# Kernel tuning notes

Measured on AMD Instinct MI355X. Metric: run time of the kernel, lower is better.

The kernel has to match this reference:

```python
import jax, jax.numpy as jnp
import numpy as np

N_NODES = 50000
N_EDGES = 800000
IN, HID, OUT = 256, 128, 64


def setup_inputs() -> dict:
    key = jax.random.key(0)
    ks = jax.random.split(key, 5)
    return {
        "x": jax.random.normal(ks[0], (N_NODES, IN), dtype=jnp.float32),
        "W1": jax.random.normal(ks[1], (IN, HID), dtype=jnp.float32) / np.sqrt(IN),
        "b1": jnp.zeros((HID,), dtype=jnp.float32),
        "W2": jax.random.normal(ks[2], (HID, OUT), dtype=jnp.float32) / np.sqrt(HID),
        "b2": jnp.zeros((OUT,), dtype=jnp.float32),
        "src": jax.random.randint(ks[3], (N_EDGES,), 0, N_NODES, dtype=jnp.int32),
        "dst": jax.random.randint(ks[4], (N_EDGES,), 0, N_NODES, dtype=jnp.int32),
    }


def _graph_conv(h, W, b, src, dst, norm_src, norm_dst, n_nodes):
    # DGL GraphConv, norm='both': y = D_dst^{-1/2} A D_src^{-1/2} h W + b
    # Project first (smaller feature dim for the SpMM), linearity makes it exact.
    h = h @ W                                     # [N, d_out]
    msg = (h * norm_src[:, None])[src]            # gather per-edge   [E, d_out]
    agg = jax.ops.segment_sum(msg, dst, num_segments=n_nodes)  # [N, d_out]
    return agg * norm_dst[:, None] + b


def reference(x, W1, b1, W2, b2, src, dst):
    n = x.shape[0]
    ones = jnp.ones(src.shape[0], dtype=jnp.float32)
    out_deg = jnp.zeros(n, jnp.float32).at[src].add(ones)
    in_deg = jnp.zeros(n, jnp.float32).at[dst].add(ones)
    norm_src = jax.lax.rsqrt(jnp.maximum(out_deg, 1.0))
    norm_dst = jax.lax.rsqrt(jnp.maximum(in_deg, 1.0))

    h = _graph_conv(x, W1, b1, src, dst, norm_src, norm_dst, n)
    h = jax.nn.relu(h)
    return _graph_conv(h, W2, b2, src, dst, norm_src, norm_dst, n)
```

## Files before the change

### kernel.cpp

```cpp
#include <hip/hip_runtime.h>

#define NN 50000
#define NE 800000
#define NPAD 50176
#define NSLICE 32
#define ESL 25000
#define HPN 25088
#define HPW 12544
#define FPN 12544
#define GB2 196
#define FB 128
#define NB 196

typedef __attribute__((ext_vector_type(8))) short bf16x8;
typedef __attribute__((ext_vector_type(4))) float f32x4;

__device__ __forceinline__ float u2f(unsigned u) { return __uint_as_float(u); }
__device__ __forceinline__ unsigned f2u(float f) { return __float_as_uint(f); }
__device__ __forceinline__ unsigned short f2bf(float f) {
    unsigned u = f2u(f);
    return (unsigned short)((u + (((u >> 16) & 1u) + 0x7fffu)) >> 16);
}
__device__ __forceinline__ void acc8(float* ax, uint4 u) {
    ax[0] += u2f(u.x << 16); ax[1] += u2f(u.x & 0xffff0000u);
    ax[2] += u2f(u.y << 16); ax[3] += u2f(u.y & 0xffff0000u);
    ax[4] += u2f(u.z << 16); ax[5] += u2f(u.z & 0xffff0000u);
    ax[6] += u2f(u.w << 16); ax[7] += u2f(u.w & 0xffff0000u);
}
#define GLOAD_LDS16(GP, LP)                                              \
    __builtin_amdgcn_global_load_lds(                                    \
        (const __attribute__((address_space(1))) unsigned*)(GP),         \
        (__attribute__((address_space(3))) unsigned*)(LP), 16, 0, 0)

__global__ __launch_bounds__(1024) void hist_wtrans_kernel(
    const int* __restrict__ src, const int* __restrict__ dst,
    unsigned* __restrict__ cnt_sl,
    const float* __restrict__ W1, const float* __restrict__ W2,
    unsigned short* __restrict__ Wh1, unsigned short* __restrict__ Wl1,
    unsigned short* __restrict__ Wh2, unsigned short* __restrict__ Wl2,
    int* __restrict__ done_cnt) {
    if (blockIdx.x == 0 && threadIdx.x == 0) *done_cnt = 0;
    const int b = blockIdx.x;
    if (b >= 128) {
        float w;
        unsigned short *ph, *pl;
        int f;
        if (b < 160) {
            int i = (b - 128) * 1024 + threadIdx.x;
            int k = i >> 7, n = i & 127;
            f = (((n >> 4) * 32 + (k >> 3)) * 16 + (n & 15)) * 8 + (k & 7);
            w = W1[i]; ph = Wh1; pl = Wl1;
        } else {
            int i = (b - 160) * 1024 + threadIdx.x;
            int k = i >> 6, n = i & 63;
            f = (((n >> 4) * 16 + (k >> 3)) * 16 + (n & 15)) * 8 + (k & 7);
            w = W2[i]; ph = Wh2; pl = Wl2;
        }
        unsigned u = f2u(w);
        float lo = w - u2f(u & 0xffff0000u);
        ph[f] = (unsigned short)(u >> 16);
        pl[f] = (unsigned short)(f2u(lo) >> 16);
        return;
    }
    __shared__ unsigned lcnt[HPW];
    const int side = b & 1;
    const int slice = (b >> 1) & (NSLICE - 1);
    const int part = b >> 6;
    const int* __restrict__ arr = side ? dst : src;
    const int base = part * HPN;
    for (int j = threadIdx.x; j < HPW; j += 1024) lcnt[j] = 0;
    __syncthreads();
    const int e0 = slice * ESL;
    for (int i = e0 + threadIdx.x; i < e0 + ESL; i += 1024) {
        int v = arr[i] - base;
        if ((unsigned)v < (unsigned)HPN)
            atomicAdd(&lcnt[v >> 1], 1u << ((v & 1) * 16));
    }
    __syncthreads();
    unsigned* o = cnt_sl + (size_t)b * HPW;
    for (int j = threadIdx.x; j < HPW; j += 1024) o[j] = lcnt[j];
}

__global__ __launch_bounds__(256) void norm_scanAB_kernel(
    const unsigned* __restrict__ cnt_sl, float* __restrict__ ns,
    float* __restrict__ nd, int* __restrict__ presum,
    int* __restrict__ pref, int* __restrict__ blk_sum,
    int* __restrict__ blk_ofs, int* __restrict__ done_cnt, int n) {
    __shared__ int lds[256];
    __shared__ int is_last;
    int i = blockIdx.x * 256 + threadIdx.x;
    int d_total = 0;
    if (i < n) {
        int part = (i >= HPN) ? 1 : 0;
        int w = (i - part * HPN) >> 1;
        int sh = (i & 1) * 16;
        int s_total = 0;
#pragma unroll
        for (int sl = 0; sl < NSLICE; sl++) {
            int bb = part * 64 + sl * 2;
            s_total += (cnt_sl[(size_t)bb * HPW + w] >> sh) & 0xffff;
            int c = (cnt_sl[(size_t)(bb + 1) * HPW + w] >> sh) & 0xffff;
            presum[sl * NPAD + i] = d_total;
            d_total += c;
        }
        ns[i] = rsqrtf(fmaxf((float)s_total, 1.0f));
        nd[i] = rsqrtf(fmaxf((float)d_total, 1.0f));
    }
    lds[threadIdx.x] = d_total;
    __syncthreads();
    for (int ofs = 1; ofs < 256; ofs <<= 1) {
        int t = (threadIdx.x >= ofs) ? lds[threadIdx.x - ofs] : 0;
        __syncthreads();
        lds[threadIdx.x] += t;
        __syncthreads();
    }
    if (i < n) pref[i] = lds[threadIdx.x] - d_total;
    if (threadIdx.x == 255) blk_sum[blockIdx.x] = lds[255];
    __threadfence();
    if (threadIdx.x == 0) {
        int c = atomicAdd(done_cnt, 1);
        is_last = (c == gridDim.x - 1);
    }
    __syncthreads();
    if (!is_last) return;
    __threadfence();
    int v = (threadIdx.x < gridDim.x) ? blk_sum[threadIdx.x] : 0;
    __syncthreads();
    lds[threadIdx.x] = v;
    __syncthreads();
    for (int ofs = 1; ofs < 256; ofs <<= 1) {
        int t = (threadIdx.x >= ofs) ? lds[threadIdx.x - ofs] : 0;
        __syncthreads();
        lds[threadIdx.x] += t;
        __syncthreads();
    }
    if (threadIdx.x < gridDim.x) blk_ofs[threadIdx.x] = lds[threadIdx.x] - v;
}

__global__ __launch_bounds__(1024) void gemm1_fill_kernel(
    const float* __restrict__ A, const unsigned short* __restrict__ Wh,
    const unsigned short* __restrict__ Wl, const float* __restrict__ norm_src,
    unsigned short* __restrict__ out,
    const int* __restrict__ src, const int* __restrict__ dst,
    const int* __restrict__ pref, const int* __restrict__ blk_ofs,
    const int* __restrict__ presum, int* __restrict__ eidx, int M) {
    __shared__ __align__(16) char shmem[65536];
    const int b = blockIdx.x;
    if (b < GB2) {
        constexpr int N = 128, K = 256;
        constexpr int NT = N / 16, KC = K / 32;
        const int wave = threadIdx.x >> 6;
        const int lane = threadIdx.x & 63;
        const int ln = lane & 15;
        const int qk = lane >> 4;
        const int m0 = b * 256 + wave * 16;
        const int m0b = b * 256;
        float* sh = (float*)shmem;
        const bf16x8* BH = (const bf16x8*)Wh;
        const bf16x8* BL = (const bf16x8*)Wl;

        auto stage = [&](int p, int c) {
#pragma unroll
            for (int h = 0; h < 2; ++h) {
                const int j = threadIdx.x + h * 1024;
                const int row = j >> 3;
                const int sp = (j & 7) ^ (row & 7);
                int grow = m0b + row;
                if (grow >= M) grow = M - 1;
                const float* gp = A + (size_t)grow * K + c * 32 + sp * 4;
                char* lp = (char*)(sh + p * 8192) + (j & ~63) * 16;
                GLOAD_LDS16(gp, lp);
            }
        };

        const int r = wave * 16 + ln;
        const int offA0 = r * 128 + (((qk * 2) ^ (ln & 7)) * 16);
        const int offA1 = r * 128 + (((qk * 2 + 1) ^ (ln & 7)) * 16);

        f32x4 acc[NT];
#pragma unroll
        for (int t = 0; t < NT; t++) acc[t] = (f32x4){0.f, 0.f, 0.f, 0.f};

        stage(0, 0);
        __syncthreads();
#pragma unroll 2
        for (int c = 0; c < KC; ++c) {
            if (c + 1 < KC) stage((c + 1) & 1, c + 1);
            const char* bufc = (const char*)sh + (c & 1) * 32768;
            float4 a0 = *(const float4*)(bufc + offA0);
            float4 a1 = *(const float4*)(bufc + offA1);
            float av[8] = {a0.x, a0.y, a0.z, a0.w, a1.x, a1.y, a1.z, a1.w};
            bf16x8 ah, al;
#pragma unroll
            for (int j = 0; j < 8; ++j) {
                unsigned u = f2u(av[j]);
                float lo = av[j] - u2f(u & 0xffff0000u);
                ah[j] = (short)(u >> 16);
                al[j] = (short)(f2u(lo) >> 16);
            }
            const int fb = c * 4 + qk;
#pragma unroll
            for (int t = 0; t < NT; ++t) {
                bf16x8 bh = BH[(t * (K / 8) + fb) * 16 + ln];
                bf16x8 bl = BL[(t * (K / 8) + fb) * 16 + ln];
                acc[t] = __builtin_amdgcn_mfma_f32_16x16x32_bf16(ah, bh, acc[t], 0, 0, 0);
                acc[t] = __builtin_amdgcn_mfma_f32_16x16x32_bf16(ah, bl, acc[t], 0, 0, 0);
                acc[t] = __builtin_amdgcn_mfma_f32_16x16x32_bf16(al, bh, acc[t], 0, 0, 0);
            }
            __syncthreads();
        }
        float sc[4];
#pragma unroll
        for (int rr = 0; rr < 4; ++rr) {
            int row = m0 + qk * 4 + rr;
            sc[rr] = (row < M) ? norm_src[row] : 0.f;
        }
#pragma unroll
        for (int t = 0; t < NT; ++t)
#pragma unroll
            for (int rr = 0; rr < 4; ++rr) {
                int row = m0 + qk * 4 + rr;
                if (row < M) out[(size_t)row * N + t * 16 + ln] = f2bf(acc[t][rr] * sc[rr]);
            }
        return;
    }
    int* cur = (int*)shmem;
    const int fb = b - GB2;
    const int slice = fb >> 2;
    const int part = fb & 3;
    const int base = part * FPN;
    for (int j = threadIdx.x; j < FPN; j += 1024) {
        int gi = base + j;
        cur[j] = (gi < NN) ? pref[gi] + blk_ofs[gi >> 8] + presum[slice * NPAD + gi] : 0;
    }
    __syncthreads();
    const int e0 = slice * ESL;
    for (int i = e0 + threadIdx.x; i < e0 + ESL; i += 1024) {
        int v = dst[i] - base;
        if ((unsigned)v < (unsigned)FPN) {
            int pos = atomicAdd(&cur[v], 1);
            eidx[pos] = src[i];
        }
    }
}

__global__ __launch_bounds__(256) void layer2_kernel(
    const unsigned* __restrict__ hs1, const int* __restrict__ eidx,
    const int* __restrict__ pref, const int* __restrict__ blk_ofs,
    const float* __restrict__ norm_src, const float* __restrict__ norm_dst,
    const float* __restrict__ bias, const unsigned short* __restrict__ Wh,
    const unsigned short* __restrict__ Wl, unsigned short* __restrict__ hs2, int n) {
    __shared__ unsigned lh1[16 * 68];
    const int wave = threadIdx.x >> 6;
    const int lane = threadIdx.x & 63;
    const int nb = blockIdx.x * 16;
    const int q = lane >> 4;
    const int p = lane & 15;

    for (int j = 0; j < 4; ++j) {
        const int node = nb + wave * 4 + j;
        float ax[8];
#pragma unroll
        for (int k = 0; k < 8; ++k) ax[k] = 0.f;
        unsigned pk[4] = {0u, 0u, 0u, 0u};
        if (node < n) {
            int beg = pref[node] + blk_ofs[node >> 8];
            int end = (node + 1 < n) ? pref[node + 1] + blk_ofs[(node + 1) >> 8] : NE;
            int e = beg;
            for (; e + 15 < end; e += 16) {
                int i0 = eidx[e + q];
                int i1 = eidx[e + 4 + q];
                int i2 = eidx[e + 8 + q];
                int i3 = eidx[e + 12 + q];
                uint4 u0 = *(const uint4*)(hs1 + (size_t)i0 * 64 + p * 4);
                uint4 u1 = *(const uint4*)(hs1 + (size_t)i1 * 64 + p * 4);
                uint4 u2 = *(const uint4*)(hs1 + (size_t)i2 * 64 + p * 4);
                uint4 u3 = *(const uint4*)(hs1 + (size_t)i3 * 64 + p * 4);
                acc8(ax, u0);
                acc8(ax, u1);
                acc8(ax, u2);
                acc8(ax, u3);
            }
            for (; e + 7 < end; e += 8) {
                int i0 = eidx[e + q];
                int i1 = eidx[e + 4 + q];
                uint4 u0 = *(const uint4*)(hs1 + (size_t)i0 * 64 + p * 4);
                uint4 u1 = *(const uint4*)(hs1 + (size_t)i1 * 64 + p * 4);
                acc8(ax, u0);
                acc8(ax, u1);
            }
            for (; e < end; e += 4) {
                int ee = e + q;
                bool ok = ee < end;
                int i0 = eidx[ok ? ee : beg];
                uint4 u0 = *(const uint4*)(hs1 + (size_t)i0 * 64 + p * 4);
                if (ok) acc8(ax, u0);
            }
#pragma unroll
            for (int k = 0; k < 8; ++k) {
                ax[k] += __shfl_xor(ax[k], 16);
                ax[k] += __shfl_xor(ax[k], 32);
            }
            float sc = norm_dst[node];
            float4 b0 = *(const float4*)(bias + p * 8);
            float4 b1 = *(const float4*)(bias + p * 8 + 4);
            float bb[8] = {b0.x, b0.y, b0.z, b0.w, b1.x, b1.y, b1.z, b1.w};
#pragma unroll
            for (int k = 0; k < 4; ++k) {
                float rlo = fmaxf(ax[2 * k] * sc + bb[2 * k], 0.f);
                float rhi = fmaxf(ax[2 * k + 1] * sc + bb[2 * k + 1], 0.f);
                pk[k] = (unsigned)f2bf(rlo) | ((unsigned)f2bf(rhi) << 16);
            }
        }
        if (q == 0)
            *(uint4*)&lh1[(wave * 4 + j) * 68 + p * 4] = *(uint4*)pk;
    }
    __syncthreads();

    const int ln = lane & 15;
    const int qk = lane >> 4;
    const int t = wave;
    const bf16x8* BH = (const bf16x8*)Wh;
    const bf16x8* BL = (const bf16x8*)Wl;
    f32x4 acc = (f32x4){0.f, 0.f, 0.f, 0.f};
#pragma unroll
    for (int c = 0; c < 4; ++c) {
        bf16x8 ah = *(const bf16x8*)&lh1[ln * 68 + c * 16 + qk * 4];
        const int fb = c * 4 + qk;
        bf16x8 bh = BH[(t * 16 + fb) * 16 + ln];
        bf16x8 bl = BL[(t * 16 + fb) * 16 + ln];
        acc = __builtin_amdgcn_mfma_f32_16x16x32_bf16(ah, bh, acc, 0, 0, 0);
        acc = __builtin_amdgcn_mfma_f32_16x16x32_bf16(ah, bl, acc, 0, 0, 0);
    }
#pragma unroll
    for (int r = 0; r < 4; ++r) {
        int node = nb + qk * 4 + r;
        if (node < n)
            hs2[(size_t)node * 64 + t * 16 + ln] = f2bf(acc[r] * norm_src[node]);
    }
}

__global__ __launch_bounds__(256) void gather64_kernel(
    const unsigned* __restrict__ hs, const int* __restrict__ eidx,
    const int* __restrict__ pref, const int* __restrict__ blk_ofs,
    const float* __restrict__ norm_dst, const float* __restrict__ bias,
    float* __restrict__ out, int n) {
    int wave = (blockIdx.x * blockDim.x + threadIdx.x) >> 6;
    int lane = threadIdx.x & 63;
    if (wave >= n) return;
    int beg = pref[wave] + blk_ofs[wave >> 8];
    int end = (wave + 1 < n) ? pref[wave + 1] + blk_ofs[(wave + 1) >> 8] : NE;
    const int o = lane >> 3;
    const int p = lane & 7;
    float ax[8];
#pragma unroll
    for (int k = 0; k < 8; ++k) ax[k] = 0.f;
    int e = beg;
    for (; e + 15 < end; e += 16) {
        int i0 = eidx[e + o];
        int i1 = eidx[e + 8 + o];
        uint4 u0 = *(const uint4*)(hs + (size_t)i0 * 32 + p * 4);
        uint4 u1 = *(const uint4*)(hs + (size_t)i1 * 32 + p * 4);
        acc8(ax, u0);
        acc8(ax, u1);
    }
    for (; e < end; e += 8) {
        int ee = e + o;
        bool ok = ee < end;
        int i0 = eidx[ok ? ee : beg];
        uint4 u0 = *(const uint4*)(hs + (size_t)i0 * 32 + p * 4);
        if (ok) acc8(ax, u0);
    }
#pragma unroll
    for (int k = 0; k < 8; ++k) {
        ax[k] += __shfl_xor(ax[k], 8);
        ax[k] += __shfl_xor(ax[k], 16);
        ax[k] += __shfl_xor(ax[k], 32);
    }
    if (o == 0) {
        float sc = norm_dst[wave];
        float4 b0 = *(const float4*)(bias + p * 8);
        float4 b1 = *(const float4*)(bias + p * 8 + 4);
        float4 r0, r1;
        r0.x = ax[0] * sc + b0.x;
        r0.y = ax[1] * sc + b0.y;
        r0.z = ax[2] * sc + b0.z;
        r0.w = ax[3] * sc + b0.w;
        r1.x = ax[4] * sc + b1.x;
        r1.y = ax[5] * sc + b1.y;
        r1.z = ax[6] * sc + b1.z;
        r1.w = ax[7] * sc + b1.w;
        *(float4*)(out + (size_t)wave * 64 + p * 8) = r0;
        *(float4*)(out + (size_t)wave * 64 + p * 8 + 4) = r1;
    }
}

extern "C" void kernel_launch(void* const* d_in, const int* in_sizes, int n_in,
                              void* d_out, int out_size, void* d_ws, size_t ws_size,
                              hipStream_t stream) {
    const float* x  = (const float*)d_in[0];
    const float* W1 = (const float*)d_in[1];
    const float* b1 = (const float*)d_in[2];
    const float* W2 = (const float*)d_in[3];
    const float* b2 = (const float*)d_in[4];
    const int* src  = (const int*)d_in[5];
    const int* dst  = (const int*)d_in[6];
    float* out = (float*)d_out;
    char* ws = (char*)d_ws;

    float* norm_src = (float*)(ws);
    float* norm_dst = (float*)(ws + 4 * 50176);
    int*   pref     = (int*)(ws + 4 * 100352);
    int*   blk_sum  = (int*)(ws + 4 * 150528);
    int*   blk_ofs  = (int*)(ws + 4 * 150784);
    int*   done_cnt = (int*)(ws + 4 * 151040);
    int*   eidx     = (int*)(ws + 4 * 151296);
    unsigned short* Wh1 = (unsigned short*)(ws + 4 * 951296);
    unsigned short* Wl1 = (unsigned short*)(ws + 4 * 967680);
    unsigned short* Wh2 = (unsigned short*)(ws + 4 * 984064);
    unsigned short* Wl2 = (unsigned short*)(ws + 4 * 988160);
    unsigned short* hs1 = (unsigned short*)(ws + 4 * 992256);
    unsigned short* hs2 = (unsigned short*)(ws + 4 * 4192256);
    unsigned* cnt_sl    = (unsigned*)(ws + 4 * 5792256);
    int* presum         = (int*)(ws + 4 * 7397888);

    hist_wtrans_kernel<<<168, 1024, 0, stream>>>(src, dst, cnt_sl, W1, W2,
                                                 Wh1, Wl1, Wh2, Wl2, done_cnt);

    norm_scanAB_kernel<<<NB, 256, 0, stream>>>(cnt_sl, norm_src, norm_dst,
                                               presum, pref, blk_sum, blk_ofs,
                                               done_cnt, NN);

    gemm1_fill_kernel<<<GB2 + FB, 1024, 0, stream>>>(
        x, Wh1, Wl1, norm_src, hs1, src, dst, pref, blk_ofs, presum, eidx, NN);

    layer2_kernel<<<3125, 256, 0, stream>>>(
        (const unsigned*)hs1, eidx, pref, blk_ofs, norm_src, norm_dst, b1,
        Wh2, Wl2, hs2, NN);

    gather64_kernel<<<12500, 256, 0, stream>>>(
        (const unsigned*)hs2, eidx, pref, blk_ofs, norm_dst, b2, out, NN);
}
```

Measured before the change: 222.4 us.

## Replace sliced LDS counting-sort fill with global atomic cursors

```diff
diff --git a/kernel.cpp b/kernel.cpp
--- a/kernel.cpp
+++ b/kernel.cpp
@@ -3,13 +3,13 @@
 #define NN 50000
 #define NE 800000
 #define NPAD 50176
-#define NSLICE 32
-#define ESL 25000
+#define NSL8 8
+#define ESL8 100000
 #define HPN 25088
 #define HPW 12544
-#define FPN 12544
 #define GB2 196
-#define FB 128
+#define FB3 59
+#define EPB 13560
 #define NB 196
 
 typedef __attribute__((ext_vector_type(8))) short bf16x8;
@@ -34,24 +34,24 @@
 
 __global__ __launch_bounds__(1024) void hist_wtrans_kernel(
     const int* __restrict__ src, const int* __restrict__ dst,
-    unsigned* __restrict__ cnt_sl,
+    unsigned* __restrict__ cnt8,
     const float* __restrict__ W1, const float* __restrict__ W2,
     unsigned short* __restrict__ Wh1, unsigned short* __restrict__ Wl1,
     unsigned short* __restrict__ Wh2, unsigned short* __restrict__ Wl2,
     int* __restrict__ done_cnt) {
     if (blockIdx.x == 0 && threadIdx.x == 0) *done_cnt = 0;
     const int b = blockIdx.x;
-    if (b >= 128) {
+    if (b >= 32) {
         float w;
         unsigned short *ph, *pl;
         int f;
-        if (b < 160) {
-            int i = (b - 128) * 1024 + threadIdx.x;
+        if (b < 64) {
+            int i = (b - 32) * 1024 + threadIdx.x;
             int k = i >> 7, n = i & 127;
             f = (((n >> 4) * 32 + (k >> 3)) * 16 + (n & 15)) * 8 + (k & 7);
             w = W1[i]; ph = Wh1; pl = Wl1;
         } else {
-            int i = (b - 160) * 1024 + threadIdx.x;
+            int i = (b - 64) * 1024 + threadIdx.x;
             int k = i >> 6, n = i & 63;
             f = (((n >> 4) * 16 + (k >> 3)) * 16 + (n & 15)) * 8 + (k & 7);
             w = W2[i]; ph = Wh2; pl = Wl2;
@@ -64,26 +64,26 @@
     }
     __shared__ unsigned lcnt[HPW];
     const int side = b & 1;
-    const int slice = (b >> 1) & (NSLICE - 1);
-    const int part = b >> 6;
+    const int slice = (b >> 1) & 7;
+    const int part = b >> 4;
     const int* __restrict__ arr = side ? dst : src;
     const int base = part * HPN;
     for (int j = threadIdx.x; j < HPW; j += 1024) lcnt[j] = 0;
     __syncthreads();
-    const int e0 = slice * ESL;
-    for (int i = e0 + threadIdx.x; i < e0 + ESL; i += 1024) {
+    const int e0 = slice * ESL8;
+    for (int i = e0 + threadIdx.x; i < e0 + ESL8; i += 1024) {
         int v = arr[i] - base;
         if ((unsigned)v < (unsigned)HPN)
             atomicAdd(&lcnt[v >> 1], 1u << ((v & 1) * 16));
     }
     __syncthreads();
-    unsigned* o = cnt_sl + (size_t)b * HPW;
+    unsigned* o = cnt8 + (size_t)b * HPW;
     for (int j = threadIdx.x; j < HPW; j += 1024) o[j] = lcnt[j];
 }
 
 __global__ __launch_bounds__(256) void norm_scanAB_kernel(
-    const unsigned* __restrict__ cnt_sl, float* __restrict__ ns,
-    float* __restrict__ nd, int* __restrict__ presum,
+    const unsigned* __restrict__ cnt8, float* __restrict__ ns,
+    float* __restrict__ nd, int* __restrict__ gcur,
     int* __restrict__ pref, int* __restrict__ blk_sum,
     int* __restrict__ blk_ofs, int* __restrict__ done_cnt, int n) {
     __shared__ int lds[256];
@@ -96,12 +96,9 @@
         int sh = (i & 1) * 16;
         int s_total = 0;
 #pragma unroll
-        for (int sl = 0; sl < NSLICE; sl++) {
-            int bb = part * 64 + sl * 2;
-            s_total += (cnt_sl[(size_t)bb * HPW + w] >> sh) & 0xffff;
-            int c = (cnt_sl[(size_t)(bb + 1) * HPW + w] >> sh) & 0xffff;
-            presum[sl * NPAD + i] = d_total;
-            d_total += c;
+        for (int sl = 0; sl < NSL8; sl++) {
+            s_total += (cnt8[(size_t)(part * 16 + sl * 2) * HPW + w] >> sh) & 0xffff;
+            d_total += (cnt8[(size_t)(part * 16 + sl * 2 + 1) * HPW + w] >> sh) & 0xffff;
         }
         ns[i] = rsqrtf(fmaxf((float)s_total, 1.0f));
         nd[i] = rsqrtf(fmaxf((float)d_total, 1.0f));
@@ -114,7 +111,11 @@
         lds[threadIdx.x] += t;
         __syncthreads();
     }
-    if (i < n) pref[i] = lds[threadIdx.x] - d_total;
+    if (i < n) {
+        int p = lds[threadIdx.x] - d_total;
+        pref[i] = p;
+        gcur[i] = p;
+    }
     if (threadIdx.x == 255) blk_sum[blockIdx.x] = lds[255];
     __threadfence();
     if (threadIdx.x == 0) {
@@ -142,8 +143,8 @@
     const unsigned short* __restrict__ Wl, const float* __restrict__ norm_src,
     unsigned short* __restrict__ out,
     const int* __restrict__ src, const int* __restrict__ dst,
-    const int* __restrict__ pref, const int* __restrict__ blk_ofs,
-    const int* __restrict__ presum, int* __restrict__ eidx, int M) {
+    int* __restrict__ gcur, const int* __restrict__ blk_ofs,
+    int* __restrict__ eidx, int M) {
     __shared__ __align__(16) char shmem[65536];
     const int b = blockIdx.x;
     if (b < GB2) {
@@ -224,23 +225,13 @@
             }
         return;
     }
-    int* cur = (int*)shmem;
     const int fb = b - GB2;
-    const int slice = fb >> 2;
-    const int part = fb & 3;
-    const int base = part * FPN;
-    for (int j = threadIdx.x; j < FPN; j += 1024) {
-        int gi = base + j;
-        cur[j] = (gi < NN) ? pref[gi] + blk_ofs[gi >> 8] + presum[slice * NPAD + gi] : 0;
-    }
-    __syncthreads();
-    const int e0 = slice * ESL;
-    for (int i = e0 + threadIdx.x; i < e0 + ESL; i += 1024) {
-        int v = dst[i] - base;
-        if ((unsigned)v < (unsigned)FPN) {
-            int pos = atomicAdd(&cur[v], 1);
-            eidx[pos] = src[i];
-        }
+    const int i0 = fb * EPB;
+    const int i1 = (i0 + EPB < NE) ? i0 + EPB : NE;
+    for (int i = i0 + threadIdx.x; i < i1; i += 1024) {
+        int v = dst[i];
+        int pos = atomicAdd(&gcur[v], 1) + blk_ofs[v >> 8];
+        eidx[pos] = src[i];
     }
 }
 
@@ -421,18 +412,18 @@
     unsigned short* Wl2 = (unsigned short*)(ws + 4 * 988160);
     unsigned short* hs1 = (unsigned short*)(ws + 4 * 992256);
     unsigned short* hs2 = (unsigned short*)(ws + 4 * 4192256);
-    unsigned* cnt_sl    = (unsigned*)(ws + 4 * 5792256);
-    int* presum         = (int*)(ws + 4 * 7397888);
-
-    hist_wtrans_kernel<<<168, 1024, 0, stream>>>(src, dst, cnt_sl, W1, W2,
-                                                 Wh1, Wl1, Wh2, Wl2, done_cnt);
-
-    norm_scanAB_kernel<<<NB, 256, 0, stream>>>(cnt_sl, norm_src, norm_dst,
-                                               presum, pref, blk_sum, blk_ofs,
+    unsigned* cnt8     = (unsigned*)(ws + 4 * 5792256);
+    int* gcur          = (int*)(ws + 4 * 7397888);
+
+    hist_wtrans_kernel<<<72, 1024, 0, stream>>>(src, dst, cnt8, W1, W2,
+                                                Wh1, Wl1, Wh2, Wl2, done_cnt);
+
+    norm_scanAB_kernel<<<NB, 256, 0, stream>>>(cnt8, norm_src, norm_dst,
+                                               gcur, pref, blk_sum, blk_ofs,
                                                done_cnt, NN);
 
-    gemm1_fill_kernel<<<GB2 + FB, 1024, 0, stream>>>(
-        x, Wh1, Wl1, norm_src, hs1, src, dst, pref, blk_ofs, presum, eidx, NN);
+    gemm1_fill_kernel<<<GB2 + FB3, 1024, 0, stream>>>(
+        x, Wh1, Wl1, norm_src, hs1, src, dst, gcur, blk_ofs, eidx, NN);
 
     layer2_kernel<<<3125, 256, 0, stream>>>(
         (const unsigned*)hs1, eidx, pref, blk_ofs, norm_src, norm_dst, b1,
```

After: 255.1 us. 1.15x slower.

## Double histogram slice blocks and schedule fill blocks before GEMM blocks

Applied to the files above, without the earlier changes.

```diff
diff --git a/kernel.cpp b/kernel.cpp
--- a/kernel.cpp
+++ b/kernel.cpp
@@ -5,11 +5,13 @@
 #define NPAD 50176
 #define NSLICE 32
 #define ESL 25000
+#define NHS 64
+#define EHS 12500
 #define HPN 25088
 #define HPW 12544
 #define FPN 12544
+#define FB 128
 #define GB2 196
-#define FB 128
 #define NB 196
 
 typedef __attribute__((ext_vector_type(8))) short bf16x8;
@@ -41,17 +43,17 @@
     int* __restrict__ done_cnt) {
     if (blockIdx.x == 0 && threadIdx.x == 0) *done_cnt = 0;
     const int b = blockIdx.x;
-    if (b >= 128) {
+    if (b >= 256) {
         float w;
         unsigned short *ph, *pl;
         int f;
-        if (b < 160) {
-            int i = (b - 128) * 1024 + threadIdx.x;
+        if (b < 288) {
+            int i = (b - 256) * 1024 + threadIdx.x;
             int k = i >> 7, n = i & 127;
             f = (((n >> 4) * 32 + (k >> 3)) * 16 + (n & 15)) * 8 + (k & 7);
             w = W1[i]; ph = Wh1; pl = Wl1;
         } else {
-            int i = (b - 160) * 1024 + threadIdx.x;
+            int i = (b - 288) * 1024 + threadIdx.x;
             int k = i >> 6, n = i & 63;
             f = (((n >> 4) * 16 + (k >> 3)) * 16 + (n & 15)) * 8 + (k & 7);
             w = W2[i]; ph = Wh2; pl = Wl2;
@@ -64,14 +66,14 @@
     }
     __shared__ unsigned lcnt[HPW];
     const int side = b & 1;
-    const int slice = (b >> 1) & (NSLICE - 1);
-    const int part = b >> 6;
+    const int slice = (b >> 1) & (NHS - 1);
+    const int part = b >> 7;
     const int* __restrict__ arr = side ? dst : src;
     const int base = part * HPN;
     for (int j = threadIdx.x; j < HPW; j += 1024) lcnt[j] = 0;
     __syncthreads();
-    const int e0 = slice * ESL;
-    for (int i = e0 + threadIdx.x; i < e0 + ESL; i += 1024) {
+    const int e0 = slice * EHS;
+    for (int i = e0 + threadIdx.x; i < e0 + EHS; i += 1024) {
         int v = arr[i] - base;
         if ((unsigned)v < (unsigned)HPN)
             atomicAdd(&lcnt[v >> 1], 1u << ((v & 1) * 16));
@@ -95,12 +97,14 @@
         int w = (i - part * HPN) >> 1;
         int sh = (i & 1) * 16;
         int s_total = 0;
-#pragma unroll
-        for (int sl = 0; sl < NSLICE; sl++) {
-            int bb = part * 64 + sl * 2;
-            s_total += (cnt_sl[(size_t)bb * HPW + w] >> sh) & 0xffff;
-            int c = (cnt_sl[(size_t)(bb + 1) * HPW + w] >> sh) & 0xffff;
-            presum[sl * NPAD + i] = d_total;
+        const int bb0 = part * 128;
+#pragma unroll
+        for (int fs = 0; fs < NSLICE; fs++) {
+            s_total += (cnt_sl[(size_t)(bb0 + 4 * fs) * HPW + w] >> sh) & 0xffff;
+            s_total += (cnt_sl[(size_t)(bb0 + 4 * fs + 2) * HPW + w] >> sh) & 0xffff;
+            int c = ((cnt_sl[(size_t)(bb0 + 4 * fs + 1) * HPW + w] >> sh) & 0xffff) +
+                    ((cnt_sl[(size_t)(bb0 + 4 * fs + 3) * HPW + w] >> sh) & 0xffff);
+            presum[fs * NPAD + i] = d_total;
             d_total += c;
         }
         ns[i] = rsqrtf(fmaxf((float)s_total, 1.0f));
@@ -146,15 +150,16 @@
     const int* __restrict__ presum, int* __restrict__ eidx, int M) {
     __shared__ __align__(16) char shmem[65536];
     const int b = blockIdx.x;
-    if (b < GB2) {
+    if (b >= FB) {
+        const int g = b - FB;
         constexpr int N = 128, K = 256;
         constexpr int NT = N / 16, KC = K / 32;
         const int wave = threadIdx.x >> 6;
         const int lane = threadIdx.x & 63;
         const int ln = lane & 15;
         const int qk = lane >> 4;
-        const int m0 = b * 256 + wave * 16;
-        const int m0b = b * 256;
+        const int m0 = g * 256 + wave * 16;
+        const int m0b = g * 256;
         float* sh = (float*)shmem;
         const bf16x8* BH = (const bf16x8*)Wh;
         const bf16x8* BL = (const bf16x8*)Wl;
@@ -198,11 +203,11 @@
                 ah[j] = (short)(u >> 16);
                 al[j] = (short)(f2u(lo) >> 16);
             }
-            const int fb = c * 4 + qk;
+            const int fb2 = c * 4 + qk;
 #pragma unroll
             for (int t = 0; t < NT; ++t) {
-                bf16x8 bh = BH[(t * (K / 8) + fb) * 16 + ln];
-                bf16x8 bl = BL[(t * (K / 8) + fb) * 16 + ln];
+                bf16x8 bh = BH[(t * (K / 8) + fb2) * 16 + ln];
+                bf16x8 bl = BL[(t * (K / 8) + fb2) * 16 + ln];
                 acc[t] = __builtin_amdgcn_mfma_f32_16x16x32_bf16(ah, bh, acc[t], 0, 0, 0);
                 acc[t] = __builtin_amdgcn_mfma_f32_16x16x32_bf16(ah, bl, acc[t], 0, 0, 0);
                 acc[t] = __builtin_amdgcn_mfma_f32_16x16x32_bf16(al, bh, acc[t], 0, 0, 0);
@@ -225,9 +230,8 @@
         return;
     }
     int* cur = (int*)shmem;
-    const int fb = b - GB2;
-    const int slice = fb >> 2;
-    const int part = fb & 3;
+    const int slice = b >> 2;
+    const int part = b & 3;
     const int base = part * FPN;
     for (int j = threadIdx.x; j < FPN; j += 1024) {
         int gi = base + j;
@@ -326,9 +330,9 @@
 #pragma unroll
     for (int c = 0; c < 4; ++c) {
         bf16x8 ah = *(const bf16x8*)&lh1[ln * 68 + c * 16 + qk * 4];
-        const int fb = c * 4 + qk;
-        bf16x8 bh = BH[(t * 16 + fb) * 16 + ln];
-        bf16x8 bl = BL[(t * 16 + fb) * 16 + ln];
+        const int fb2 = c * 4 + qk;
+        bf16x8 bh = BH[(t * 16 + fb2) * 16 + ln];
+        bf16x8 bl = BL[(t * 16 + fb2) * 16 + ln];
         acc = __builtin_amdgcn_mfma_f32_16x16x32_bf16(ah, bh, acc, 0, 0, 0);
         acc = __builtin_amdgcn_mfma_f32_16x16x32_bf16(ah, bl, acc, 0, 0, 0);
     }
@@ -422,16 +426,16 @@
     unsigned short* hs1 = (unsigned short*)(ws + 4 * 992256);
     unsigned short* hs2 = (unsigned short*)(ws + 4 * 4192256);
     unsigned* cnt_sl    = (unsigned*)(ws + 4 * 5792256);
-    int* presum         = (int*)(ws + 4 * 7397888);
-
-    hist_wtrans_kernel<<<168, 1024, 0, stream>>>(src, dst, cnt_sl, W1, W2,
+    int* presum         = (int*)(ws + 4 * 9003520);
+
+    hist_wtrans_kernel<<<296, 1024, 0, stream>>>(src, dst, cnt_sl, W1, W2,
                                                  Wh1, Wl1, Wh2, Wl2, done_cnt);
 
     norm_scanAB_kernel<<<NB, 256, 0, stream>>>(cnt_sl, norm_src, norm_dst,
                                                presum, pref, blk_sum, blk_ofs,
                                                done_cnt, NN);
 
-    gemm1_fill_kernel<<<GB2 + FB, 1024, 0, stream>>>(
+    gemm1_fill_kernel<<<FB + GB2, 1024, 0, stream>>>(
         x, Wh1, Wl1, norm_src, hs1, src, dst, pref, blk_ofs, presum, eidx, NN);
 
     layer2_kernel<<<3125, 256, 0, stream>>>(
```

Result: no change. 223.7 us (+0.6%).
